# Performance work log

Hardware: AMD Instinct MI355X
Metric: run time of the kernel (lower is better)

Reference implementation:

```python
import jax, jax.numpy as jnp
import numpy as np

B, N, D = 2, 2048, 1024
RANK, HEADS = 256, 16
HS = RANK // HEADS          # 16, low-rank head size for QK
DH = D // HEADS             # 64, value head size
SCALE = 1.0 / np.sqrt(HS)


def setup_inputs() -> dict:
    key = jax.random.key(0)
    k1, k2, k3 = jax.random.split(key, 3)
    x = jax.random.normal(k1, (B, N, D), dtype=jnp.float32)
    # causal additive mask, 0 on/below diag, -1e9 above
    mask = jnp.where(jnp.tril(jnp.ones((N, N), dtype=bool)), 0.0, -1e9).astype(jnp.float32)
    Wqk = jax.random.normal(k2, (2 * RANK, D), dtype=jnp.float32) * (1.0 / np.sqrt(D))
    Wv = jax.random.normal(k3, (D, D), dtype=jnp.float32) * (1.0 / np.sqrt(D))
    return {"x": x, "mask": mask, "Wqk": Wqk, "Wv": Wv}


def reference(x, mask, Wqk, Wv):
    b, n, d = x.shape
    qk = jnp.einsum('bnd,rd->bnr', x, Wqk)            # [b,n,2*rank]
    q, k = jnp.split(qk, 2, axis=-1)                  # [b,n,rank] each
    # L2 normalize over FULL rank dim (before head split), clamp norm >= 1e-6
    q = q / jnp.maximum(jnp.linalg.norm(q, axis=-1, keepdims=True), 1e-6)
    k = k / jnp.maximum(jnp.linalg.norm(k, axis=-1, keepdims=True), 1e-6)
    q = q.reshape(b, n, HEADS, HS).transpose(0, 2, 1, 3)   # [b,h,n,hs]
    k = k.reshape(b, n, HEADS, HS).transpose(0, 2, 1, 3)
    v = jnp.einsum('bnd,ed->bne', x, Wv).reshape(b, n, HEADS, DH).transpose(0, 2, 1, 3)  # [b,h,n,dh]
    att = jnp.einsum('bhqe,bhke->bhqk', q, k) * SCALE
    att = jnp.clip(att, -10000.0, 10000.0)
    att = att + mask[None, None, :, :]
    att = jax.nn.softmax(att, axis=-1)
    # NaN guard: zero NaNs then renormalize (no-op when no NaNs)
    att = jnp.where(jnp.isnan(att), 0.0, att)
    att = att / jnp.maximum(att.sum(axis=-1, keepdims=True), 1e-6)
    y = jnp.einsum('bhqk,bhkd->bhqd', att, v)              # [b,h,n,dh]
    return y.transpose(0, 2, 1, 3).reshape(b, n, d)
```

## Files before the change

kernel.cpp:

```cpp
#include <hip/hip_runtime.h>
#include <math.h>

#define BATCH 2
#define SEQ   2048
#define DIM   1024
#define RANK  256
#define HEADS 16
#define HS    16
#define DH    64
#define MROWS 4096

#define QSCALE 0.36067376f

typedef __attribute__((ext_vector_type(8)))  short    short8;
typedef __attribute__((ext_vector_type(4)))  float    f32x4;
typedef __attribute__((ext_vector_type(16))) float    f32x16;
typedef __attribute__((ext_vector_type(2)))  unsigned uint2v;

__device__ __forceinline__ unsigned short f2bf(float f) {
    union { float f; unsigned u; } v; v.f = f;
    return (unsigned short)((v.u + 0x7FFFu + ((v.u >> 16) & 1u)) >> 16);
}
__device__ __forceinline__ float bf2f(unsigned short h) {
    union { unsigned u; float f; } v; v.u = ((unsigned)h) << 16;
    return v.f;
}

#define XQ   1048576
#define WQKQ 131072
#define WVQ  262144
__global__ __launch_bounds__(256) void conv3(const float* __restrict__ x,
                                             const float* __restrict__ wqk,
                                             const float* __restrict__ wv,
                                             unsigned short* __restrict__ xb,
                                             unsigned short* __restrict__ wcat)
{
    const int i = blockIdx.x * 256 + threadIdx.x;
    const float* src; unsigned short* dst; int j;
    if (i < XQ)              { src = x;   dst = xb;   j = i; }
    else if (i < XQ + WQKQ)  { src = wqk; dst = wcat; j = i - XQ; }
    else                     { src = wv;  dst = wcat + (size_t)4 * WQKQ; j = i - XQ - WQKQ; }
    float4 v = ((const float4*)src)[j];
    ushort4 o; o.x = f2bf(v.x); o.y = f2bf(v.y); o.z = f2bf(v.z); o.w = f2bf(v.w);
    ((ushort4*)dst)[j] = o;
}

__global__ __launch_bounds__(256) void gemm_mfma(const unsigned short* __restrict__ A,
                                                 const unsigned short* __restrict__ W,
                                                 unsigned short* __restrict__ qkb,
                                                 unsigned short* __restrict__ vt)
{
    __shared__ __align__(16) unsigned short Alds[128 * 32];
    __shared__ __align__(16) unsigned short Blds[64 * 32];

    const int tid = threadIdx.x;
    const int w = tid >> 6, lane = tid & 63;
    const int lr = lane & 15, lg = lane >> 4;
    const int wm = w >> 1, wn = w & 1;
    const int bm = blockIdx.x * 128, bn = blockIdx.y * 64;

    const int srow = lane >> 2;
    const int sk   = (lane & 3) * 8;

    f32x4 acc[4][2] = {};

    for (int k0 = 0; k0 < 1024; k0 += 32) {
        __syncthreads();
        #pragma unroll
        for (int q = 0; q < 2; ++q) {
            const int r = (w * 2 + q) * 16 + srow;
            __builtin_amdgcn_global_load_lds(
                (const __attribute__((address_space(1))) unsigned int*)&A[(size_t)(bm + r) * 1024 + k0 + sk],
                (__attribute__((address_space(3))) unsigned int*)&Alds[(w * 2 + q) * 512],
                16, 0, 0);
        }
        __builtin_amdgcn_global_load_lds(
            (const __attribute__((address_space(1))) unsigned int*)&W[(size_t)(bn + w * 16 + srow) * 1024 + k0 + sk],
            (__attribute__((address_space(3))) unsigned int*)&Blds[w * 512],
            16, 0, 0);
        __syncthreads();

        short8 af[4], bfr[2];
        #pragma unroll
        for (int mi = 0; mi < 4; ++mi)
            af[mi] = *(const short8*)&Alds[(wm * 64 + mi * 16 + lr) * 32 + lg * 8];
        #pragma unroll
        for (int ni = 0; ni < 2; ++ni)
            bfr[ni] = *(const short8*)&Blds[(wn * 32 + ni * 16 + lr) * 32 + lg * 8];
        #pragma unroll
        for (int mi = 0; mi < 4; ++mi)
            #pragma unroll
            for (int ni = 0; ni < 2; ++ni)
                acc[mi][ni] = __builtin_amdgcn_mfma_f32_16x16x32_bf16(af[mi], bfr[ni], acc[mi][ni], 0, 0, 0);
    }

    if (bn < 512) {
        #pragma unroll
        for (int mi = 0; mi < 4; ++mi) {
            const int rbase = bm + wm * 64 + mi * 16 + lg * 4;
            #pragma unroll
            for (int ni = 0; ni < 2; ++ni) {
                const int col = bn + wn * 32 + ni * 16 + lr;
                #pragma unroll
                for (int r = 0; r < 4; ++r)
                    qkb[(size_t)(rbase + r) * 512 + col] = f2bf(acc[mi][ni][r]);
            }
        }
    } else {
        const int nb = bn - 512;
        #pragma unroll
        for (int mi = 0; mi < 4; ++mi) {
            const int m = bm + wm * 64 + mi * 16 + lg * 4;
            const int bb = m >> 11, ms = m & 2047;
            #pragma unroll
            for (int ni = 0; ni < 2; ++ni) {
                const int d = nb + wn * 32 + ni * 16 + lr;
                ushort4 pk;
                pk.x = f2bf(acc[mi][ni][0]); pk.y = f2bf(acc[mi][ni][1]);
                pk.z = f2bf(acc[mi][ni][2]); pk.w = f2bf(acc[mi][ni][3]);
                *(ushort4*)&vt[((size_t)bb * DIM + d) * SEQ + ms] = pk;
            }
        }
    }
}

__global__ __launch_bounds__(256) void l2norm_split(const unsigned short* __restrict__ qkb,
                                                    unsigned short* __restrict__ qn,
                                                    unsigned short* __restrict__ kn)
{
    const int row = blockIdx.x;
    const int t = threadIdx.x;
    const unsigned short* p = qkb + (size_t)row * 512;
    float q = bf2f(p[t]);
    float k = bf2f(p[t + 256]);
    float sq = q * q, sk = k * k;
    #pragma unroll
    for (int off = 32; off > 0; off >>= 1) {
        sq += __shfl_down(sq, off);
        sk += __shfl_down(sk, off);
    }
    __shared__ float sh[8];
    const int wid = t >> 6;
    if ((t & 63) == 0) { sh[wid * 2] = sq; sh[wid * 2 + 1] = sk; }
    __syncthreads();
    sq = sh[0] + sh[2] + sh[4] + sh[6];
    sk = sh[1] + sh[3] + sh[5] + sh[7];
    const float rq = QSCALE / fmaxf(sqrtf(sq), 1e-6f);
    const float rk = 1.0f   / fmaxf(sqrtf(sk), 1e-6f);
    qn[(size_t)row * 256 + t] = f2bf(q * rq);
    kn[(size_t)row * 256 + t] = f2bf(k * rk);
}


template<bool MASK>
__device__ __forceinline__ void tile32(const unsigned short* Vs, int keybase, int kh,
                                       int l31, int hi, int qg,
                                       const short8 ak0, const short8 ak1, const short8 bq,
                                       f32x16 o[2], float& lpart)
{
    const f32x16 z = {};
    const f32x16 s0 = __builtin_amdgcn_mfma_f32_32x32x16_bf16(ak0, bq, z, 0, 0, 0);
    const f32x16 s1 = __builtin_amdgcn_mfma_f32_32x32x16_bf16(ak1, bq, z, 0, 0, 0);

    float p0[16], p1[16];
    #pragma unroll
    for (int r = 0; r < 16; ++r) {
        float e0 = __builtin_exp2f(s0[r]);
        float e1 = __builtin_exp2f(s1[r]);
        if (MASK) {
            const int kl = keybase + (r & 3) + 8 * (r >> 2) + 4 * hi;
            e0 = (kl > qg) ? 0.0f : e0;
            e1 = (kl + 32 > qg) ? 0.0f : e1;
        }
        p0[r] = e0; p1[r] = e1;
        lpart += e0 + e1;
    }

    short8 pa[4];
    #pragma unroll
    for (int g = 0; g < 4; ++g) {
        const float* pc = (g < 2) ? p0 : p1;
        const int jj = 2 * (g & 1);
        unsigned a0, a1, b0, b1;
        asm("v_cvt_pk_bf16_f32 %0, %1, %2" : "=v"(a0) : "v"(pc[4*jj]),     "v"(pc[4*jj + 1]));
        asm("v_cvt_pk_bf16_f32 %0, %1, %2" : "=v"(b0) : "v"(pc[4*jj + 2]), "v"(pc[4*jj + 3]));
        asm("v_cvt_pk_bf16_f32 %0, %1, %2" : "=v"(a1) : "v"(pc[4*jj + 4]), "v"(pc[4*jj + 5]));
        asm("v_cvt_pk_bf16_f32 %0, %1, %2" : "=v"(b1) : "v"(pc[4*jj + 6]), "v"(pc[4*jj + 7]));
        const uint2v r0 = __builtin_amdgcn_permlane32_swap(a0, a1, false, false);
        const uint2v r1 = __builtin_amdgcn_permlane32_swap(b0, b1, false, false);
        union { short8 s; unsigned u[4]; } pu;
        pu.u[0] = r0[0]; pu.u[1] = r1[0]; pu.u[2] = r0[1]; pu.u[3] = r1[1];
        pa[g] = pu.s;
    }

    #pragma unroll
    for (int g = 0; g < 4; ++g)
        #pragma unroll
        for (int half = 0; half < 2; ++half) {
            const int row = half * 32 + l31;
            const short8 bv = *(const short8*)&Vs[row * 128 + ((64 * kh + 16 * g + 8 * hi) ^ (8 * (row & 7)))];
            o[half] = __builtin_amdgcn_mfma_f32_32x32x16_bf16(pa[g], bv, o[half], 0, 0, 0);
        }
}

__device__ __forceinline__ void seg_tile(const unsigned short* Vs, int kb, int kh,
                                         int l31, int hi, int qband, int qg, bool last,
                                         const short8 ak0, const short8 ak1, const short8 bq,
                                         f32x16 o[2], float& lpart)
{
    if (!last) {
        tile32<false>(Vs, kb, kh, l31, hi, qg, ak0, ak1, bq, o, lpart);
    } else if (kb <= qband + 31) {
        if (kb + 63 <= qband)
            tile32<false>(Vs, kb, kh, l31, hi, qg, ak0, ak1, bq, o, lpart);
        else
            tile32<true>(Vs, kb, kh, l31, hi, qg, ak0, ak1, bq, o, lpart);
    }
}

__global__ __launch_bounds__(256, 2) void attn_pair(const unsigned short* __restrict__ qn,
                                                    const unsigned short* __restrict__ kn,
                                                    const unsigned short* __restrict__ vt,
                                                    float* __restrict__ out)
{
    const int L = blockIdx.x;
    const int bh = L & 31;
    const int p  = L >> 5;
    const int h = bh & 15, b = bh >> 4;

    const int tid = threadIdx.x, w = tid >> 6, lane = tid & 63;
    const int qh = w >> 1, kh = w & 1;
    const int l31 = lane & 31, hi = lane >> 5;

    const int qt0 = 31 - p, qt1 = p;
    const int nt0 = (qt0 >> 1) + 1;
    const int nt1 = (qt1 >> 1) + 1;
    const int qband0 = qt0 * 64 + qh * 32, qband1 = qt1 * 64 + qh * 32;
    const int qg0 = qband0 + l31, qg1 = qband1 + l31;

    __shared__ __align__(16) unsigned char smem[33792];

    const short8 bq0 = *(const short8*)&qn[((size_t)b * SEQ + qg0) * RANK + h * HS + 8 * hi];
    const short8 bq1 = *(const short8*)&qn[((size_t)b * SEQ + qg1) * RANK + h * HS + 8 * hi];

    f32x16 o0[2] = {}, o1[2] = {};
    float lp0 = 0.0f, lp1 = 0.0f;

    const unsigned short* kbase = kn + ((size_t)b * SEQ + 64 * kh + l31) * RANK + h * HS + 8 * hi;
    short8 ak0 = *(const short8*)kbase;
    short8 ak1 = *(const short8*)(kbase + 32 * RANK);

    const int vsub  = lane >> 4;
    const int vslot = lane & 15;

#define STAGEV(kt_, buf_) do {                                                                    \
        const int k0_ = (kt_) * 128;                                                              \
        _Pragma("unroll")                                                                         \
        for (int i = 0; i < 4; ++i) {                                                             \
            const int dh = w * 16 + i * 4 + vsub;                                                 \
            const int so = 8 * (vslot ^ (dh & 7));                                                \
            __builtin_amdgcn_global_load_lds(                                                     \
                (const __attribute__((address_space(1))) unsigned int*)                           \
                    &vt[((size_t)b * DIM + h * DH + dh) * SEQ + k0_ + so],                        \
                (__attribute__((address_space(3))) unsigned int*)(smem + (buf_) * 16384 + (w * 4 + i) * 1024), \
                16, 0, 0);                                                                        \
        }                                                                                         \
    } while (0)

    STAGEV(0, 0);
    __syncthreads();

    #pragma unroll 1
    for (int kt = 0; kt < nt0; ++kt) {
        const bool more = (kt + 1 < nt0);
        if (more) STAGEV(kt + 1, (kt + 1) & 1);
        short8 an0 = ak0, an1 = ak1;
        if (more) {
            an0 = *(const short8*)(kbase + (size_t)(kt + 1) * 128 * RANK);
            an1 = *(const short8*)(kbase + (size_t)(kt + 1) * 128 * RANK + 32 * RANK);
        }

        const unsigned short* Vs = (const unsigned short*)(smem + (kt & 1) * 16384);
        const int kb = kt * 128 + 64 * kh;

        __builtin_amdgcn_s_setprio(1);
        seg_tile(Vs, kb, kh, l31, hi, qband0, qg0, kt == nt0 - 1, ak0, ak1, bq0, o0, lp0);
        if (kt < nt1)
            seg_tile(Vs, kb, kh, l31, hi, qband1, qg1, kt == nt1 - 1, ak0, ak1, bq1, o1, lp1);
        __builtin_amdgcn_s_setprio(0);

        ak0 = an0; ak1 = an1;
        __syncthreads();
    }
#undef STAGEV

    float* Os0 = (float*)smem;
    float* Os1 = (float*)(smem + 16384);
    float* Ls0 = (float*)(smem + 32768);
    float* Ls1 = (float*)(smem + 33280);

    if (kh == 1) {
        #pragma unroll
        for (int half = 0; half < 2; ++half)
            #pragma unroll
            for (int r = 0; r < 16; ++r) {
                const int q = (r & 3) + 8 * (r >> 2) + 4 * hi;
                Os0[(qh * 32 + q) * 64 + half * 32 + l31] = o0[half][r];
                Os1[(qh * 32 + q) * 64 + half * 32 + l31] = o1[half][r];
            }
        Ls0[qh * 64 + lane] = lp0;
        Ls1[qh * 64 + lane] = lp1;
    }
    __syncthreads();
    if (kh == 0) {
        float lt0 = lp0 + Ls0[qh * 64 + lane];
        float lt1 = lp1 + Ls1[qh * 64 + lane];
        lt0 += __shfl_xor(lt0, 32);
        lt1 += __shfl_xor(lt1, 32);
        const float inv0 = 1.0f / fmaxf(lt0, 1e-6f);
        const float inv1 = 1.0f / fmaxf(lt1, 1e-6f);
        #pragma unroll
        for (int r = 0; r < 16; ++r) {
            const int q = (r & 3) + 8 * (r >> 2) + 4 * hi;
            const float iv0 = __shfl(inv0, q);
            const float iv1 = __shfl(inv1, q);
            #pragma unroll
            for (int half = 0; half < 2; ++half) {
                const float v0 = (o0[half][r] + Os0[(qh * 32 + q) * 64 + half * 32 + l31]) * iv0;
                const float v1 = (o1[half][r] + Os1[(qh * 32 + q) * 64 + half * 32 + l31]) * iv1;
                __builtin_nontemporal_store(v0,
                    &out[((size_t)b * SEQ + qband0 + q) * DIM + h * DH + half * 32 + l31]);
                __builtin_nontemporal_store(v1,
                    &out[((size_t)b * SEQ + qband1 + q) * DIM + h * DH + half * 32 + l31]);
            }
        }
    }
}

extern "C" void kernel_launch(void* const* d_in, const int* in_sizes, int n_in,
                              void* d_out, int out_size, void* d_ws, size_t ws_size,
                              hipStream_t stream)
{
    const float* x   = (const float*)d_in[0];
    const float* Wqk = (const float*)d_in[2];
    const float* Wv  = (const float*)d_in[3];
    float* out = (float*)d_out;

    unsigned short* xb   = (unsigned short*)d_ws;
    unsigned short* qkb  = xb  + (size_t)MROWS * DIM;
    unsigned short* vt   = qkb + (size_t)MROWS * 512;
    unsigned short* wcat = vt  + (size_t)BATCH * DIM * SEQ;
    unsigned short* qn = xb;
    unsigned short* kn = xb + (size_t)MROWS * RANK;

    conv3<<<5632, 256, 0, stream>>>(x, Wqk, Wv, xb, wcat);
    gemm_mfma<<<dim3(32, 24), 256, 0, stream>>>(xb, wcat, qkb, vt);
    l2norm_split<<<MROWS, 256, 0, stream>>>(qkb, qn, kn);
    attn_pair<<<dim3(512), 256, 0, stream>>>(qn, kn, vt, out);
}
```

Before: 73.29 us.

## Split attention into 32-row band pairs with 4-way key split; swizzle GEMM LDS

The attention kernel now uses 32-query bands paired as (63-j, j), 1024 blocks, and four waves that each take a 32-key quarter of every 128-key tile. Partial outputs and row sums are reduced across the four waves through LDS. Occupancy is raised to four blocks per CU to improve load balance and latency hiding. The projection GEMM uses a K-step of 64 with XOR-swizzled LDS layout and a remapped 1D grid order for better L2 locality, at the cost of more reduction and sync traffic in the attention epilogue.

```diff
diff --git a/kernel.cpp b/kernel.cpp
--- a/kernel.cpp
+++ b/kernel.cpp
@@ -17,6 +17,9 @@
 typedef __attribute__((ext_vector_type(16))) float    f32x16;
 typedef __attribute__((ext_vector_type(2)))  unsigned uint2v;
 
+#define GPTR const __attribute__((address_space(1))) unsigned int*
+#define LPTR __attribute__((address_space(3))) unsigned int*
+
 __device__ __forceinline__ unsigned short f2bf(float f) {
     union { float f; unsigned u; } v; v.f = f;
     return (unsigned short)((v.u + 0x7FFFu + ((v.u >> 16) & 1u)) >> 16);
@@ -50,48 +53,60 @@
                                                  unsigned short* __restrict__ qkb,
                                                  unsigned short* __restrict__ vt)
 {
-    __shared__ __align__(16) unsigned short Alds[128 * 32];
-    __shared__ __align__(16) unsigned short Blds[64 * 32];
+    __shared__ __align__(16) unsigned short Alds[128 * 64];
+    __shared__ __align__(16) unsigned short Blds[64 * 64];
 
     const int tid = threadIdx.x;
     const int w = tid >> 6, lane = tid & 63;
     const int lr = lane & 15, lg = lane >> 4;
     const int wm = w >> 1, wn = w & 1;
-    const int bm = blockIdx.x * 128, bn = blockIdx.y * 64;
-
-    const int srow = lane >> 2;
-    const int sk   = (lane & 3) * 8;
+
+    const int Lf = blockIdx.x;
+    const int wg = (Lf & 7) * 96 + (Lf >> 3);
+    const int bm = (wg & 31) * 128;
+    const int bn = (wg >> 5) * 64;
+
+    const int rs = lane >> 3, cs = lane & 7;
 
     f32x4 acc[4][2] = {};
 
-    for (int k0 = 0; k0 < 1024; k0 += 32) {
+    for (int k0 = 0; k0 < 1024; k0 += 64) {
         __syncthreads();
         #pragma unroll
-        for (int q = 0; q < 2; ++q) {
-            const int r = (w * 2 + q) * 16 + srow;
+        for (int i = 0; i < 4; ++i) {
+            const int r = w * 32 + i * 8 + rs;
             __builtin_amdgcn_global_load_lds(
-                (const __attribute__((address_space(1))) unsigned int*)&A[(size_t)(bm + r) * 1024 + k0 + sk],
-                (__attribute__((address_space(3))) unsigned int*)&Alds[(w * 2 + q) * 512],
-                16, 0, 0);
-        }
-        __builtin_amdgcn_global_load_lds(
-            (const __attribute__((address_space(1))) unsigned int*)&W[(size_t)(bn + w * 16 + srow) * 1024 + k0 + sk],
-            (__attribute__((address_space(3))) unsigned int*)&Blds[w * 512],
-            16, 0, 0);
+                (GPTR)&A[(size_t)(bm + r) * 1024 + k0 + 8 * (cs ^ (r & 7))],
+                (LPTR)&Alds[(w * 32 + i * 8) * 64], 16, 0, 0);
+        }
+        #pragma unroll
+        for (int i = 0; i < 2; ++i) {
+            const int r = w * 16 + i * 8 + rs;
+            __builtin_amdgcn_global_load_lds(
+                (GPTR)&W[(size_t)(bn + r) * 1024 + k0 + 8 * (cs ^ (r & 7))],
+                (LPTR)&Blds[(w * 16 + i * 8) * 64], 16, 0, 0);
+        }
         __syncthreads();
 
-        short8 af[4], bfr[2];
-        #pragma unroll
-        for (int mi = 0; mi < 4; ++mi)
-            af[mi] = *(const short8*)&Alds[(wm * 64 + mi * 16 + lr) * 32 + lg * 8];
-        #pragma unroll
-        for (int ni = 0; ni < 2; ++ni)
-            bfr[ni] = *(const short8*)&Blds[(wn * 32 + ni * 16 + lr) * 32 + lg * 8];
-        #pragma unroll
-        for (int mi = 0; mi < 4; ++mi)
-            #pragma unroll
-            for (int ni = 0; ni < 2; ++ni)
-                acc[mi][ni] = __builtin_amdgcn_mfma_f32_16x16x32_bf16(af[mi], bfr[ni], acc[mi][ni], 0, 0, 0);
+        #pragma unroll
+        for (int kk = 0; kk < 2; ++kk) {
+            short8 af[4], bfr[2];
+            #pragma unroll
+            for (int mi = 0; mi < 4; ++mi) {
+                const int row = wm * 64 + mi * 16 + lr;
+                af[mi] = *(const short8*)&Alds[row * 64 + 8 * ((kk * 4 + lg) ^ (row & 7))];
+            }
+            #pragma unroll
+            for (int ni = 0; ni < 2; ++ni) {
+                const int row = wn * 32 + ni * 16 + lr;
+                bfr[ni] = *(const short8*)&Blds[row * 64 + 8 * ((kk * 4 + lg) ^ (row & 7))];
+            }
+            #pragma unroll
+            for (int mi = 0; mi < 4; ++mi)
+                #pragma unroll
+                for (int ni = 0; ni < 2; ++ni)
+                    acc[mi][ni] = __builtin_amdgcn_mfma_f32_16x16x32_bf16(af[mi], bfr[ni], acc[mi][ni], 0, 0, 0);
+        }
     }
 
     if (bn < 512) {
@@ -153,39 +168,35 @@
 
 
 template<bool MASK>
-__device__ __forceinline__ void tile32(const unsigned short* Vs, int keybase, int kh,
-                                       int l31, int hi, int qg,
-                                       const short8 ak0, const short8 ak1, const short8 bq,
-                                       f32x16 o[2], float& lpart)
+__device__ __forceinline__ void tile_bp(const unsigned short* Vs, int kb, int kh,
+                                        int l31, int hi, int qg,
+                                        const short8 ak, const short8 bq,
+                                        f32x16 o[2], float& lp)
 {
     const f32x16 z = {};
-    const f32x16 s0 = __builtin_amdgcn_mfma_f32_32x32x16_bf16(ak0, bq, z, 0, 0, 0);
-    const f32x16 s1 = __builtin_amdgcn_mfma_f32_32x32x16_bf16(ak1, bq, z, 0, 0, 0);
-
-    float p0[16], p1[16];
+    const f32x16 s = __builtin_amdgcn_mfma_f32_32x32x16_bf16(ak, bq, z, 0, 0, 0);
+
+    float p[16];
     #pragma unroll
     for (int r = 0; r < 16; ++r) {
-        float e0 = __builtin_exp2f(s0[r]);
-        float e1 = __builtin_exp2f(s1[r]);
+        float e = __builtin_exp2f(s[r]);
         if (MASK) {
-            const int kl = keybase + (r & 3) + 8 * (r >> 2) + 4 * hi;
-            e0 = (kl > qg) ? 0.0f : e0;
-            e1 = (kl + 32 > qg) ? 0.0f : e1;
-        }
-        p0[r] = e0; p1[r] = e1;
-        lpart += e0 + e1;
-    }
-
-    short8 pa[4];
+            const int kl = kb + (r & 3) + 8 * (r >> 2) + 4 * hi;
+            e = (kl > qg) ? 0.0f : e;
+        }
+        p[r] = e;
+        lp += e;
+    }
+
+    short8 pa[2];
     #pragma unroll
-    for (int g = 0; g < 4; ++g) {
-        const float* pc = (g < 2) ? p0 : p1;
-        const int jj = 2 * (g & 1);
+    for (int g = 0; g < 2; ++g) {
+        const int jj = 2 * g;
         unsigned a0, a1, b0, b1;
-        asm("v_cvt_pk_bf16_f32 %0, %1, %2" : "=v"(a0) : "v"(pc[4*jj]),     "v"(pc[4*jj + 1]));
-        asm("v_cvt_pk_bf16_f32 %0, %1, %2" : "=v"(b0) : "v"(pc[4*jj + 2]), "v"(pc[4*jj + 3]));
-        asm("v_cvt_pk_bf16_f32 %0, %1, %2" : "=v"(a1) : "v"(pc[4*jj + 4]), "v"(pc[4*jj + 5]));
-        asm("v_cvt_pk_bf16_f32 %0, %1, %2" : "=v"(b1) : "v"(pc[4*jj + 6]), "v"(pc[4*jj + 7]));
+        asm("v_cvt_pk_bf16_f32 %0, %1, %2" : "=v"(a0) : "v"(p[4*jj]),     "v"(p[4*jj + 1]));
+        asm("v_cvt_pk_bf16_f32 %0, %1, %2" : "=v"(b0) : "v"(p[4*jj + 2]), "v"(p[4*jj + 3]));
+        asm("v_cvt_pk_bf16_f32 %0, %1, %2" : "=v"(a1) : "v"(p[4*jj + 4]), "v"(p[4*jj + 5]));
+        asm("v_cvt_pk_bf16_f32 %0, %1, %2" : "=v"(b1) : "v"(p[4*jj + 6]), "v"(p[4*jj + 7]));
         const uint2v r0 = __builtin_amdgcn_permlane32_swap(a0, a1, false, false);
         const uint2v r1 = __builtin_amdgcn_permlane32_swap(b0, b1, false, false);
         union { short8 s; unsigned u[4]; } pu;
@@ -194,51 +205,50 @@
     }
 
     #pragma unroll
-    for (int g = 0; g < 4; ++g)
+    for (int g = 0; g < 2; ++g)
         #pragma unroll
         for (int half = 0; half < 2; ++half) {
             const int row = half * 32 + l31;
-            const short8 bv = *(const short8*)&Vs[row * 128 + ((64 * kh + 16 * g + 8 * hi) ^ (8 * (row & 7)))];
+            const int slot = (4 * kh + 2 * g + hi) ^ (row & 15);
+            const short8 bv = *(const short8*)&Vs[row * 128 + 8 * slot];
             o[half] = __builtin_amdgcn_mfma_f32_32x32x16_bf16(pa[g], bv, o[half], 0, 0, 0);
         }
 }
 
-__device__ __forceinline__ void seg_tile(const unsigned short* Vs, int kb, int kh,
-                                         int l31, int hi, int qband, int qg, bool last,
-                                         const short8 ak0, const short8 ak1, const short8 bq,
-                                         f32x16 o[2], float& lpart)
+__device__ __forceinline__ void seg_dispatch(const unsigned short* Vs, int kb, int kh,
+                                             int l31, int hi, int band, int qg, bool last,
+                                             const short8 ak, const short8 bq,
+                                             f32x16 o[2], float& lp)
 {
     if (!last) {
-        tile32<false>(Vs, kb, kh, l31, hi, qg, ak0, ak1, bq, o, lpart);
-    } else if (kb <= qband + 31) {
-        if (kb + 63 <= qband)
-            tile32<false>(Vs, kb, kh, l31, hi, qg, ak0, ak1, bq, o, lpart);
+        tile_bp<false>(Vs, kb, kh, l31, hi, qg, ak, bq, o, lp);
+    } else if (kb <= band * 32 + 31) {
+        if (kb + 31 <= band * 32)
+            tile_bp<false>(Vs, kb, kh, l31, hi, qg, ak, bq, o, lp);
         else
-            tile32<true>(Vs, kb, kh, l31, hi, qg, ak0, ak1, bq, o, lpart);
-    }
-}
-
-__global__ __launch_bounds__(256, 2) void attn_pair(const unsigned short* __restrict__ qn,
-                                                    const unsigned short* __restrict__ kn,
-                                                    const unsigned short* __restrict__ vt,
-                                                    float* __restrict__ out)
+            tile_bp<true>(Vs, kb, kh, l31, hi, qg, ak, bq, o, lp);
+    }
+}
+
+__global__ __launch_bounds__(256, 4) void attn_bp(const unsigned short* __restrict__ qn,
+                                                  const unsigned short* __restrict__ kn,
+                                                  const unsigned short* __restrict__ vt,
+                                                  float* __restrict__ out)
 {
     const int L = blockIdx.x;
     const int bh = L & 31;
-    const int p  = L >> 5;
+    const int j  = L >> 5;
     const int h = bh & 15, b = bh >> 4;
 
-    const int tid = threadIdx.x, w = tid >> 6, lane = tid & 63;
-    const int qh = w >> 1, kh = w & 1;
+    const int tid = threadIdx.x, kh = tid >> 6, lane = tid & 63;
     const int l31 = lane & 31, hi = lane >> 5;
 
-    const int qt0 = 31 - p, qt1 = p;
-    const int nt0 = (qt0 >> 1) + 1;
-    const int nt1 = (qt1 >> 1) + 1;
-    const int qband0 = qt0 * 64 + qh * 32, qband1 = qt1 * 64 + qh * 32;
-    const int qg0 = qband0 + l31, qg1 = qband1 + l31;
-
-    __shared__ __align__(16) unsigned char smem[33792];
+    const int band0 = 63 - j, band1 = j;
+    const int nt0 = (band0 >> 2) + 1;
+    const int nt1 = (band1 >> 2) + 1;
+    const int qg0 = band0 * 32 + l31, qg1 = band1 * 32 + l31;
+
+    __shared__ __align__(16) unsigned char smem[32768 + 2048];
 
     const short8 bq0 = *(const short8*)&qn[((size_t)b * SEQ + qg0) * RANK + h * HS + 8 * hi];
     const short8 bq1 = *(const short8*)&qn[((size_t)b * SEQ + qg1) * RANK + h * HS + 8 * hi];
@@ -246,9 +256,8 @@
     f32x16 o0[2] = {}, o1[2] = {};
     float lp0 = 0.0f, lp1 = 0.0f;
 
-    const unsigned short* kbase = kn + ((size_t)b * SEQ + 64 * kh + l31) * RANK + h * HS + 8 * hi;
-    short8 ak0 = *(const short8*)kbase;
-    short8 ak1 = *(const short8*)(kbase + 32 * RANK);
+    const unsigned short* kpbase = kn + ((size_t)b * SEQ + 32 * kh + l31) * RANK + h * HS + 8 * hi;
+    short8 ak = *(const short8*)kpbase;
 
     const int vsub  = lane >> 4;
     const int vslot = lane & 15;
@@ -257,13 +266,11 @@
         const int k0_ = (kt_) * 128;                                                              \
         _Pragma("unroll")                                                                         \
         for (int i = 0; i < 4; ++i) {                                                             \
-            const int dh = w * 16 + i * 4 + vsub;                                                 \
-            const int so = 8 * (vslot ^ (dh & 7));                                                \
+            const int dh = kh * 16 + i * 4 + vsub;                                                \
+            const int so = 8 * (vslot ^ (dh & 15));                                               \
             __builtin_amdgcn_global_load_lds(                                                     \
-                (const __attribute__((address_space(1))) unsigned int*)                           \
-                    &vt[((size_t)b * DIM + h * DH + dh) * SEQ + k0_ + so],                        \
-                (__attribute__((address_space(3))) unsigned int*)(smem + (buf_) * 16384 + (w * 4 + i) * 1024), \
-                16, 0, 0);                                                                        \
+                (GPTR)&vt[((size_t)b * DIM + h * DH + dh) * SEQ + k0_ + so],                      \
+                (LPTR)(smem + (buf_) * 16384 + (kh * 16 + i * 4) * 256), 16, 0, 0);               \
         }                                                                                         \
     } while (0)
 
@@ -274,49 +281,71 @@
     for (int kt = 0; kt < nt0; ++kt) {
         const bool more = (kt + 1 < nt0);
         if (more) STAGEV(kt + 1, (kt + 1) & 1);
-        short8 an0 = ak0, an1 = ak1;
-        if (more) {
-            an0 = *(const short8*)(kbase + (size_t)(kt + 1) * 128 * RANK);
-            an1 = *(const short8*)(kbase + (size_t)(kt + 1) * 128 * RANK + 32 * RANK);
-        }
+        short8 an = ak;
+        if (more) an = *(const short8*)(kpbase + (size_t)(kt + 1) * 128 * RANK);
 
         const unsigned short* Vs = (const unsigned short*)(smem + (kt & 1) * 16384);
-        const int kb = kt * 128 + 64 * kh;
+        const int kb = kt * 128 + 32 * kh;
 
         __builtin_amdgcn_s_setprio(1);
-        seg_tile(Vs, kb, kh, l31, hi, qband0, qg0, kt == nt0 - 1, ak0, ak1, bq0, o0, lp0);
+        seg_dispatch(Vs, kb, kh, l31, hi, band0, qg0, kt == nt0 - 1, ak, bq0, o0, lp0);
         if (kt < nt1)
-            seg_tile(Vs, kb, kh, l31, hi, qband1, qg1, kt == nt1 - 1, ak0, ak1, bq1, o1, lp1);
+            seg_dispatch(Vs, kb, kh, l31, hi, band1, qg1, kt == nt1 - 1, ak, bq1, o1, lp1);
         __builtin_amdgcn_s_setprio(0);
 
-        ak0 = an0; ak1 = an1;
+        ak = an;
         __syncthreads();
     }
 #undef STAGEV
 
-    float* Os0 = (float*)smem;
-    float* Os1 = (float*)(smem + 16384);
-    float* Ls0 = (float*)(smem + 32768);
-    float* Ls1 = (float*)(smem + 33280);
-
-    if (kh == 1) {
+    lp0 += __shfl_xor(lp0, 32);
+    lp1 += __shfl_xor(lp1, 32);
+
+    float* Os = (float*)smem;
+    float* Ls = (float*)(smem + 32768);
+
+    __syncthreads();
+    Ls[(0 * 4 + kh) * 64 + lane] = lp0;
+    Ls[(1 * 4 + kh) * 64 + lane] = lp1;
+    if (kh >= 2) {
+        const int slot = kh - 2;
         #pragma unroll
         for (int half = 0; half < 2; ++half)
             #pragma unroll
             for (int r = 0; r < 16; ++r) {
                 const int q = (r & 3) + 8 * (r >> 2) + 4 * hi;
-                Os0[(qh * 32 + q) * 64 + half * 32 + l31] = o0[half][r];
-                Os1[(qh * 32 + q) * 64 + half * 32 + l31] = o1[half][r];
-            }
-        Ls0[qh * 64 + lane] = lp0;
-        Ls1[qh * 64 + lane] = lp1;
+                Os[((slot * 2 + 0) * 32 + q) * 64 + half * 32 + l31] = o0[half][r];
+                Os[((slot * 2 + 1) * 32 + q) * 64 + half * 32 + l31] = o1[half][r];
+            }
+    }
+    __syncthreads();
+    if (kh < 2) {
+        #pragma unroll
+        for (int half = 0; half < 2; ++half)
+            #pragma unroll
+            for (int r = 0; r < 16; ++r) {
+                const int q = (r & 3) + 8 * (r >> 2) + 4 * hi;
+                o0[half][r] += Os[((kh * 2 + 0) * 32 + q) * 64 + half * 32 + l31];
+                o1[half][r] += Os[((kh * 2 + 1) * 32 + q) * 64 + half * 32 + l31];
+            }
+    }
+    __syncthreads();
+    if (kh == 1) {
+        #pragma unroll
+        for (int half = 0; half < 2; ++half)
+            #pragma unroll
+            for (int r = 0; r < 16; ++r) {
+                const int q = (r & 3) + 8 * (r >> 2) + 4 * hi;
+                Os[((0 * 2 + 0) * 32 + q) * 64 + half * 32 + l31] = o0[half][r];
+                Os[((0 * 2 + 1) * 32 + q) * 64 + half * 32 + l31] = o1[half][r];
+            }
     }
     __syncthreads();
     if (kh == 0) {
-        float lt0 = lp0 + Ls0[qh * 64 + lane];
-        float lt1 = lp1 + Ls1[qh * 64 + lane];
-        lt0 += __shfl_xor(lt0, 32);
-        lt1 += __shfl_xor(lt1, 32);
+        float lt0 = Ls[(0 * 4 + 0) * 64 + lane] + Ls[(0 * 4 + 1) * 64 + lane]
+                  + Ls[(0 * 4 + 2) * 64 + lane] + Ls[(0 * 4 + 3) * 64 + lane];
+        float lt1 = Ls[(1 * 4 + 0) * 64 + lane] + Ls[(1 * 4 + 1) * 64 + lane]
+                  + Ls[(1 * 4 + 2) * 64 + lane] + Ls[(1 * 4 + 3) * 64 + lane];
         const float inv0 = 1.0f / fmaxf(lt0, 1e-6f);
         const float inv1 = 1.0f / fmaxf(lt1, 1e-6f);
         #pragma unroll
@@ -326,12 +355,12 @@
             const float iv1 = __shfl(inv1, q);
             #pragma unroll
             for (int half = 0; half < 2; ++half) {
-                const float v0 = (o0[half][r] + Os0[(qh * 32 + q) * 64 + half * 32 + l31]) * iv0;
-                const float v1 = (o1[half][r] + Os1[(qh * 32 + q) * 64 + half * 32 + l31]) * iv1;
+                const float v0 = (o0[half][r] + Os[((0 * 2 + 0) * 32 + q) * 64 + half * 32 + l31]) * iv0;
+                const float v1 = (o1[half][r] + Os[((0 * 2 + 1) * 32 + q) * 64 + half * 32 + l31]) * iv1;
                 __builtin_nontemporal_store(v0,
-                    &out[((size_t)b * SEQ + qband0 + q) * DIM + h * DH + half * 32 + l31]);
+                    &out[((size_t)b * SEQ + band0 * 32 + q) * DIM + h * DH + half * 32 + l31]);
                 __builtin_nontemporal_store(v1,
-                    &out[((size_t)b * SEQ + qband1 + q) * DIM + h * DH + half * 32 + l31]);
+                    &out[((size_t)b * SEQ + band1 * 32 + q) * DIM + h * DH + half * 32 + l31]);
             }
         }
     }
@@ -354,7 +383,7 @@
     unsigned short* kn = xb + (size_t)MROWS * RANK;
 
     conv3<<<5632, 256, 0, stream>>>(x, Wqk, Wv, xb, wcat);
-    gemm_mfma<<<dim3(32, 24), 256, 0, stream>>>(xb, wcat, qkb, vt);
+    gemm_mfma<<<768, 256, 0, stream>>>(xb, wcat, qkb, vt);
     l2norm_split<<<MROWS, 256, 0, stream>>>(qkb, qn, kn);
-    attn_pair<<<dim3(512), 256, 0, stream>>>(qn, kn, vt, out);
-}
+    attn_bp<<<1024, 256, 0, stream>>>(qn, kn, vt, out);
+}
```

Result: slower. 126.0 us (+71.9%).
